# Kernel optimization log

Measured on AMD Instinct MI355X. Metric: run time of the kernel, lower is better.

Reference implementation:

```python
import jax, jax.numpy as jnp
import numpy as np


def setup_inputs() -> dict:
    key = jax.random.key(0)
    ks = jax.random.split(key, 6)
    B, S, DK = 4, 2048, 1024
    scale = 1.0 / np.sqrt(DK)  # keep weight magnitudes sane like torch init
    return {
        "q": jax.random.normal(ks[0], (B, S, DK), jnp.float32),
        "k": jax.random.normal(ks[1], (B, S, DK), jnp.float32),
        "v": jax.random.normal(ks[2], (B, S, DK), jnp.float32),
        "wq": jax.random.normal(ks[3], (DK, DK), jnp.float32) * scale,
        "wk": jax.random.normal(ks[4], (DK, DK), jnp.float32) * scale,
        "wv": jax.random.normal(ks[5], (DK, DK), jnp.float32) * scale,
    }


def reference(q, k, v, wq, wk, wv):
    dk = q.shape[-1]
    # nn.Linear: y = x @ W^T  (weights stored [out, in])
    qp = jnp.einsum("bsd,ed->bse", q, wq)
    kp = jnp.einsum("bsd,ed->bse", k, wk)
    vp = jnp.einsum("bsd,ed->bse", v, wv)
    norm = 1.0 / jnp.sqrt(jnp.asarray(dk, qp.dtype))
    s = jnp.einsum("bqd,bkd->bqk", qp, kp) * norm  # [B, S, S]
    # module computes exp(s)/sum(exp(s)) manually; mathematically softmax
    e = jnp.exp(s)
    attention = e / jnp.sum(e, axis=-1, keepdims=True)
    # dropout is identity in eval mode (deterministic reference)
    return jnp.einsum("bqk,bkd->bqd", attention, vp)
```

## Files before the change

kernel.cpp:

```cpp
#include <hip/hip_runtime.h>

typedef _Float16 f16;
typedef _Float16 f16x4 __attribute__((ext_vector_type(4)));
typedef _Float16 f16x8 __attribute__((ext_vector_type(8)));
typedef float    fx4   __attribute__((ext_vector_type(4)));

#define MODE_PROJ   0
#define MODE_SCORES 1
#define MODE_PV     2

constexpr int Bsz = 4;
constexpr int S   = 2048;
constexpr int DK  = 1024;
constexpr int BM = 128, BN = 128, BK = 64;
constexpr long SD   = (long)S * DK;
constexpr long SS   = (long)S * S;
constexpr long BIGN = (long)Bsz * S * DK;

__device__ __forceinline__ void glds16(const f16* g, f16* l) {
    __builtin_amdgcn_global_load_lds(
        (const __attribute__((address_space(1))) void*)g,
        (__attribute__((address_space(3))) void*)l, 16, 0, 0);
}

__global__ __launch_bounds__(256)
void wconvert_kernel(const float* wq, const float* wk, const float* wv,
                     f16* wqh, f16* wkh, f16* wvh, float* rowsum)
{
    int bx = blockIdx.x;
    if (bx < 1536) {
        int t = bx >> 9, blk = bx & 511;
        const float* src = (t == 0) ? wq : (t == 1) ? wk : wv;
        f16*         dst = (t == 0) ? wqh : (t == 1) ? wkh : wvh;
        size_t off = (size_t)blk * 2048 + (size_t)threadIdx.x * 8;
        float4 f0 = *(const float4*)(src + off);
        float4 f1 = *(const float4*)(src + off + 4);
        f16x8 h = {(f16)f0.x, (f16)f0.y, (f16)f0.z, (f16)f0.w,
                   (f16)f1.x, (f16)f1.y, (f16)f1.z, (f16)f1.w};
        *(f16x8*)(dst + off) = h;
    } else {
        int blk = bx - 1536;
        size_t off = (size_t)blk * 2048 + (size_t)threadIdx.x * 8;
        fx4 z4 = {0.f, 0.f, 0.f, 0.f};
        *(fx4*)(rowsum + off)     = z4;
        *(fx4*)(rowsum + off + 4) = z4;
    }
}

template<int MODE>
__global__ __launch_bounds__(256, 3)
void gemm_kernel(const float* Fq, const float* Fk, const float* Fv,
                 const f16* B0, const f16* B1, const f16* B2,
                 const f16* A0,
                 void* O0, void* O1, float* rowsum,
                 int lda, int ldb, int K, int ldo)
{
    __shared__ f16 lA[BM * BK];
    __shared__ f16 lB[BN * BK];

    const int tid = threadIdx.x;
    const int id  = blockIdx.x;
    const int z   = blockIdx.y;
    int row0, col0;
    if constexpr (MODE == MODE_PROJ) { row0 = (id & 63) * BM; col0 = (id >> 6) * BN; }
    else                             { row0 = (id & 15) * BM; col0 = (id >> 4) * BN; }

    const int lane = tid & 63;
    const int quad = lane >> 4;
    const int cn   = lane & 15;
    const int w    = tid >> 6;
    const int wm   = w >> 1;
    const int wn   = w & 1;

    const float* Afp = nullptr;
    const f16 *Ap = nullptr, *Bp;
    if constexpr (MODE == MODE_PROJ) {
        Afp = (z == 0) ? Fq : (z == 1) ? Fk : Fv;
        Bp  = (z == 0) ? B0 : (z == 1) ? B1 : B2;
    } else if constexpr (MODE == MODE_SCORES) {
        Ap = A0 + (long)z * SD;  Bp = B0 + (long)z * SD;
        rowsum += (long)z * S;
    } else {
        Ap = A0 + (long)z * SS;  Bp = B0 + (long)z * SD;
        rowsum += (long)z * S;
    }

    fx4 acc[4][4];
    #pragma unroll
    for (int mt = 0; mt < 4; ++mt)
        #pragma unroll
        for (int nt = 0; nt < 4; ++nt)
            acc[mt][nt] = (fx4){0.f, 0.f, 0.f, 0.f};

    const int lr8 = lane >> 3;
    const int lcS = ((lane & 7) ^ lr8) << 3;

    for (int k0 = 0; k0 < K; k0 += BK) {
        __syncthreads();
        if constexpr (MODE == MODE_PROJ) {
            #pragma unroll
            for (int i = 0; i < 4; ++i) {
                int rb = w * 32 + i * 8;
                glds16(Bp + (size_t)(col0 + rb + lr8) * ldb + k0 + lcS, &lB[rb * BK]);
            }
            #pragma unroll
            for (int i = 0; i < 4; ++i) {
                int idx = tid + i * 256;
                int r   = idx >> 3;
                int ch  = idx & 7;
                const float* src = Afp + (size_t)(row0 + r) * lda + k0 + ch * 8;
                float4 a0 = *(const float4*)src;
                float4 a1 = *(const float4*)(src + 4);
                f16x8 h = {(f16)a0.x, (f16)a0.y, (f16)a0.z, (f16)a0.w,
                           (f16)a1.x, (f16)a1.y, (f16)a1.z, (f16)a1.w};
                *(f16x8*)&lA[r * BK + ((ch ^ (r & 7)) << 3)] = h;
            }
        } else {
            #pragma unroll
            for (int i = 0; i < 4; ++i) {
                int rb = w * 32 + i * 8;
                glds16(Ap + (size_t)(row0 + rb + lr8) * lda + k0 + lcS, &lA[rb * BK]);
                glds16(Bp + (size_t)(col0 + rb + lr8) * ldb + k0 + lcS, &lB[rb * BK]);
            }
        }
        __syncthreads();

        #pragma unroll
        for (int kh = 0; kh < 2; ++kh) {
            f16x8 af[4], bf[4];
            #pragma unroll
            for (int mt = 0; mt < 4; ++mt) {
                int r = wm * 64 + mt * 16 + cn;
                int ch = ((kh << 2) | quad) ^ (r & 7);
                af[mt] = *(const f16x8*)&lA[r * BK + ch * 8];
            }
            #pragma unroll
            for (int nt = 0; nt < 4; ++nt) {
                int r = wn * 64 + nt * 16 + cn;
                int ch = ((kh << 2) | quad) ^ (r & 7);
                bf[nt] = *(const f16x8*)&lB[r * BK + ch * 8];
            }
            #pragma unroll
            for (int mt = 0; mt < 4; ++mt)
                #pragma unroll
                for (int nt = 0; nt < 4; ++nt)
                    acc[mt][nt] = __builtin_amdgcn_mfma_f32_16x16x32_f16(
                        af[mt], bf[nt], acc[mt][nt], 0, 0, 0);
        }
    }

    if constexpr (MODE == MODE_PROJ) {
        if (z < 2) {
            f16* O = (f16*)O0 + (long)z * BIGN;
            #pragma unroll
            for (int mt = 0; mt < 4; ++mt) {
                int r0 = row0 + wm * 64 + mt * 16 + quad * 4;
                #pragma unroll
                for (int nt = 0; nt < 4; ++nt) {
                    int c = col0 + wn * 64 + nt * 16 + cn;
                    #pragma unroll
                    for (int reg = 0; reg < 4; ++reg)
                        O[(size_t)(r0 + reg) * DK + c] = (f16)acc[mt][nt][reg];
                }
            }
        } else {
            #pragma unroll
            for (int mt = 0; mt < 4; ++mt) {
                int r0 = row0 + wm * 64 + mt * 16 + quad * 4;
                int b  = r0 >> 11;
                int s  = r0 & 2047;
                f16* O = (f16*)O1 + (long)b * SD;
                #pragma unroll
                for (int nt = 0; nt < 4; ++nt) {
                    int c = col0 + wn * 64 + nt * 16 + cn;
                    f16x4 h = {(f16)acc[mt][nt][0], (f16)acc[mt][nt][1],
                               (f16)acc[mt][nt][2], (f16)acc[mt][nt][3]};
                    *(f16x4*)&O[(size_t)c * S + s] = h;
                }
            }
        }
    } else if constexpr (MODE == MODE_SCORES) {
        f16* O = (f16*)O0 + (long)z * SS;
        const float sl2e = 0.03125f * 1.44269504f;
        float rs[4][4];
        #pragma unroll
        for (int mt = 0; mt < 4; ++mt)
            #pragma unroll
            for (int reg = 0; reg < 4; ++reg) rs[mt][reg] = 0.f;
        #pragma unroll
        for (int mt = 0; mt < 4; ++mt) {
            int r0 = row0 + wm * 64 + mt * 16 + quad * 4;
            #pragma unroll
            for (int nt = 0; nt < 4; ++nt) {
                int c = col0 + wn * 64 + nt * 16 + cn;
                #pragma unroll
                for (int reg = 0; reg < 4; ++reg) {
                    float vv = exp2f(acc[mt][nt][reg] * sl2e);
                    rs[mt][reg] += vv;
                    O[(size_t)(r0 + reg) * ldo + c] = (f16)vv;
                }
            }
        }
        #pragma unroll
        for (int mt = 0; mt < 4; ++mt) {
            int r0 = row0 + wm * 64 + mt * 16 + quad * 4;
            #pragma unroll
            for (int reg = 0; reg < 4; ++reg) {
                float vv = rs[mt][reg];
                vv += __shfl_xor(vv, 1);
                vv += __shfl_xor(vv, 2);
                vv += __shfl_xor(vv, 4);
                vv += __shfl_xor(vv, 8);
                if (cn == 0) atomicAdd(&rowsum[r0 + reg], vv);
            }
        }
    } else {
        float* O = (float*)O0 + (long)z * SD;
        #pragma unroll
        for (int mt = 0; mt < 4; ++mt) {
            int r0 = row0 + wm * 64 + mt * 16 + quad * 4;
            fx4 rsv = *(const fx4*)&rowsum[r0];
            fx4 inv = {1.f / rsv[0], 1.f / rsv[1], 1.f / rsv[2], 1.f / rsv[3]};
            #pragma unroll
            for (int nt = 0; nt < 4; ++nt) {
                int c = col0 + wn * 64 + nt * 16 + cn;
                #pragma unroll
                for (int reg = 0; reg < 4; ++reg)
                    O[(size_t)(r0 + reg) * ldo + c] = acc[mt][nt][reg] * inv[reg];
            }
        }
    }
}

extern "C" void kernel_launch(void* const* d_in, const int* in_sizes, int n_in,
                              void* d_out, int out_size, void* d_ws, size_t ws_size,
                              hipStream_t stream) {
    const float* q  = (const float*)d_in[0];
    const float* k  = (const float*)d_in[1];
    const float* v  = (const float*)d_in[2];
    const float* wq = (const float*)d_in[3];
    const float* wk = (const float*)d_in[4];
    const float* wv = (const float*)d_in[5];
    float* out = (float*)d_out;

    char* ws = (char*)d_ws;
    f16*   qp     = (f16*)(ws);
    f16*   kp     = (f16*)(ws + ((size_t)16 << 20));
    f16*   vpT    = (f16*)(ws + ((size_t)32 << 20));
    f16*   E      = (f16*)(ws + ((size_t)48 << 20));
    float* rowsum = (float*)(ws + ((size_t)80 << 20));
    f16*   wqh    = (f16*)(ws + ((size_t)81 << 20));
    f16*   wkh    = (f16*)(ws + ((size_t)83 << 20));
    f16*   wvh    = (f16*)(ws + ((size_t)85 << 20));

    wconvert_kernel<<<1540, 256, 0, stream>>>(wq, wk, wv, wqh, wkh, wvh, rowsum);

    dim3 blk(256);
    gemm_kernel<MODE_PROJ><<<dim3(512, 3), blk, 0, stream>>>(
        q, k, v, wqh, wkh, wvh, nullptr, qp, vpT, nullptr, DK, DK, DK, DK);
    gemm_kernel<MODE_SCORES><<<dim3(256, 4), blk, 0, stream>>>(
        nullptr, nullptr, nullptr, kp, nullptr, nullptr, qp, E, nullptr, rowsum,
        DK, DK, DK, S);
    gemm_kernel<MODE_PV><<<dim3(128, 4), blk, 0, stream>>>(
        nullptr, nullptr, nullptr, vpT, nullptr, nullptr, E, out, nullptr, rowsum,
        S, S, S, DK);
}
```

Baseline: 314.8 us.

## Load fp32 projection activations directly into LDS and convert at fragment read

In the projection GEMM, the fp32 A tile is now copied into shared memory with async global-to-LDS loads, using a swizzled fp32 layout. It is converted to fp16 only when each MFMA fragment is read, instead of going through registers and converting before the LDS store. The aim is to drop the register-staged load/convert/store path and its VGPR pressure. In exchange the projection LDS footprint grows to 48KB and the fp32-to-fp16 conversion is repeated per fragment read. The scores and PV kernels now use a shared char buffer and a min-blocks launch bound of 4 instead of 3.

```diff
diff --git a/kernel.cpp b/kernel.cpp
--- a/kernel.cpp
+++ b/kernel.cpp
@@ -17,7 +17,7 @@
 constexpr long SS   = (long)S * S;
 constexpr long BIGN = (long)Bsz * S * DK;
 
-__device__ __forceinline__ void glds16(const f16* g, f16* l) {
+__device__ __forceinline__ void glds16(const void* g, void* l) {
     __builtin_amdgcn_global_load_lds(
         (const __attribute__((address_space(1))) void*)g,
         (__attribute__((address_space(3))) void*)l, 16, 0, 0);
@@ -48,15 +48,17 @@
 }
 
 template<int MODE>
-__global__ __launch_bounds__(256, 3)
+__global__ __launch_bounds__(256, MODE == MODE_PROJ ? 3 : 4)
 void gemm_kernel(const float* Fq, const float* Fk, const float* Fv,
                  const f16* B0, const f16* B1, const f16* B2,
                  const f16* A0,
                  void* O0, void* O1, float* rowsum,
                  int lda, int ldb, int K, int ldo)
 {
-    __shared__ f16 lA[BM * BK];
-    __shared__ f16 lB[BN * BK];
+    __shared__ __align__(16) char smem[MODE == MODE_PROJ ? 49152 : 32768];
+    float* lAf = (float*)smem;
+    f16*   lAh = (f16*)smem;
+    f16*   lB  = (f16*)(smem + (MODE == MODE_PROJ ? 32768 : 16384));
 
     const int tid = threadIdx.x;
     const int id  = blockIdx.x;
@@ -94,6 +96,8 @@
 
     const int lr8 = lane >> 3;
     const int lcS = ((lane & 7) ^ lr8) << 3;
+    const int lr4 = lane >> 4;
+    const int ch16 = lane & 15;
 
     for (int k0 = 0; k0 < K; k0 += BK) {
         __syncthreads();
@@ -104,22 +108,17 @@
                 glds16(Bp + (size_t)(col0 + rb + lr8) * ldb + k0 + lcS, &lB[rb * BK]);
             }
             #pragma unroll
-            for (int i = 0; i < 4; ++i) {
-                int idx = tid + i * 256;
-                int r   = idx >> 3;
-                int ch  = idx & 7;
-                const float* src = Afp + (size_t)(row0 + r) * lda + k0 + ch * 8;
-                float4 a0 = *(const float4*)src;
-                float4 a1 = *(const float4*)(src + 4);
-                f16x8 h = {(f16)a0.x, (f16)a0.y, (f16)a0.z, (f16)a0.w,
-                           (f16)a1.x, (f16)a1.y, (f16)a1.z, (f16)a1.w};
-                *(f16x8*)&lA[r * BK + ((ch ^ (r & 7)) << 3)] = h;
+            for (int i = 0; i < 8; ++i) {
+                int rb = w * 32 + i * 4;
+                int r  = rb + lr4;
+                int gc = ch16 ^ (2 * (r & 7));
+                glds16(Afp + (size_t)(row0 + r) * lda + k0 + gc * 4, &lAf[rb * BK]);
             }
         } else {
             #pragma unroll
             for (int i = 0; i < 4; ++i) {
                 int rb = w * 32 + i * 8;
-                glds16(Ap + (size_t)(row0 + rb + lr8) * lda + k0 + lcS, &lA[rb * BK]);
+                glds16(Ap + (size_t)(row0 + rb + lr8) * lda + k0 + lcS, &lAh[rb * BK]);
                 glds16(Bp + (size_t)(col0 + rb + lr8) * ldb + k0 + lcS, &lB[rb * BK]);
             }
         }
@@ -131,8 +130,17 @@
             #pragma unroll
             for (int mt = 0; mt < 4; ++mt) {
                 int r = wm * 64 + mt * 16 + cn;
-                int ch = ((kh << 2) | quad) ^ (r & 7);
-                af[mt] = *(const f16x8*)&lA[r * BK + ch * 8];
+                if constexpr (MODE == MODE_PROJ) {
+                    int pc = (kh * 8 + quad * 2) ^ (2 * (r & 7));
+                    const float* p = &lAf[r * BK + pc * 4];
+                    float4 lo = *(const float4*)p;
+                    float4 hi = *(const float4*)(p + 4);
+                    af[mt] = (f16x8){(f16)lo.x, (f16)lo.y, (f16)lo.z, (f16)lo.w,
+                                     (f16)hi.x, (f16)hi.y, (f16)hi.z, (f16)hi.w};
+                } else {
+                    int ch = ((kh << 2) | quad) ^ (r & 7);
+                    af[mt] = *(const f16x8*)&lAh[r * BK + ch * 8];
+                }
             }
             #pragma unroll
             for (int nt = 0; nt < 4; ++nt) {
```

Measured after the change: 373.3 us. 18.6% more time.
